# Performance work log

Measured on AMD Instinct MI355X. Metric: run time of the kernel, lower is better.

## Reference

```python
import jax, jax.numpy as jnp
import numpy as np

NUM_BITS = 8
SEQ, BATCH, INPUT, HIDDEN = 512, 256, 256, 256


def fake_quant(w):
    # symmetric per-tensor uniform fake-quantization with straight-through estimator
    qmax = 2.0 ** (NUM_BITS - 1) - 1.0
    scale = jnp.max(jnp.abs(w)) / qmax
    wq = jnp.round(w / scale) * scale
    return w + jax.lax.stop_gradient(wq - w)


def gru_cell(x, h, w_ih, w_hh, b_ih, b_hh):
    # x: [B, I], h: [B, H]; w_ih: [3H, I], w_hh: [3H, H]
    gi = x @ fake_quant(w_ih).T + b_ih  # [B, 3H]
    gh = h @ fake_quant(w_hh).T + b_hh  # [B, 3H]
    i_r, i_z, i_n = jnp.split(gi, 3, axis=-1)
    h_r, h_z, h_n = jnp.split(gh, 3, axis=-1)
    r = jax.nn.sigmoid(i_r + h_r)
    z = jax.nn.sigmoid(i_z + h_z)
    n = jnp.tanh(i_n + r * h_n)
    return (1.0 - z) * n + z * h


def setup_inputs() -> dict:
    key = jax.random.key(0)
    ks = jax.random.split(key, 9)
    s1 = 1.0 / np.sqrt(HIDDEN)
    inp = {
        "x": jax.random.normal(ks[0], (SEQ, BATCH, INPUT), dtype=jnp.float32),
        "h1": jnp.zeros((BATCH, HIDDEN), dtype=jnp.float32),
        "h2": jnp.zeros((BATCH, HIDDEN), dtype=jnp.float32),
        "w_ih1": jax.random.uniform(ks[1], (3 * HIDDEN, INPUT), jnp.float32, -s1, s1),
        "w_hh1": jax.random.uniform(ks[2], (3 * HIDDEN, HIDDEN), jnp.float32, -s1, s1),
        "b_ih1": jax.random.uniform(ks[3], (3 * HIDDEN,), jnp.float32, -s1, s1),
        "b_hh1": jax.random.uniform(ks[4], (3 * HIDDEN,), jnp.float32, -s1, s1),
        "w_ih2": jax.random.uniform(ks[5], (3 * HIDDEN, HIDDEN), jnp.float32, -s1, s1),
        "w_hh2": jax.random.uniform(ks[6], (3 * HIDDEN, HIDDEN), jnp.float32, -s1, s1),
        "b_ih2": jax.random.uniform(ks[7], (3 * HIDDEN,), jnp.float32, -s1, s1),
        "b_hh2": jax.random.uniform(ks[8], (3 * HIDDEN,), jnp.float32, -s1, s1),
    }
    return inp


def reference(x, h1, h2, w_ih1, w_hh1, b_ih1, b_hh1, w_ih2, w_hh2, b_ih2, b_hh2):
    def step(carry, x_t):
        h1, h2 = carry
        h1 = gru_cell(x_t, h1, w_ih1, w_hh1, b_ih1, b_hh1)
        h2 = gru_cell(h1, h2, w_ih2, w_hh2, b_ih2, b_hh2)
        return (h1, h2), None

    (h1, h2), _ = jax.lax.scan(step, (h1, h2), x)
    return h2
```

## Files before the change

kernel.cpp:

```cpp
#include <hip/hip_runtime.h>
#include <hip/hip_fp16.h>
#include <cstdint>

typedef _Float16 half8 __attribute__((ext_vector_type(8)));
typedef _Float16 half4 __attribute__((ext_vector_type(4)));
typedef float f32x4 __attribute__((ext_vector_type(4)));

#define MFMA_F16 __builtin_amdgcn_mfma_f32_16x16x32_f16
#define PIN(x)   asm volatile("" : "+v"(x))
#define LD_RLX(p)   __hip_atomic_load((p),  __ATOMIC_RELAXED, __HIP_MEMORY_SCOPE_AGENT)
#define LD_ACQ(p)   __hip_atomic_load((p),  __ATOMIC_ACQUIRE, __HIP_MEMORY_SCOPE_AGENT)
#define ST_REL(p,v) __hip_atomic_store((p),(v), __ATOMIC_RELEASE, __HIP_MEMORY_SCOPE_AGENT)

__device__ __forceinline__ float fast_rcp(float x){
#if __has_builtin(__builtin_amdgcn_rcpf)
  return __builtin_amdgcn_rcpf(x);
#else
  return 1.0f/x;
#endif
}
__device__ __forceinline__ float fast_exp2(float x){
#if __has_builtin(__builtin_amdgcn_exp2f)
  return __builtin_amdgcn_exp2f(x);
#else
  return exp2f(x);
#endif
}
__device__ __forceinline__ float sigm_f(float x){
  return fast_rcp(1.0f + fast_exp2(-1.44269504f*x));
}
__device__ __forceinline__ float tanh_fast(float x){
  float e = fast_exp2(-2.88539008f*x);
  return fmaf(2.0f, fast_rcp(1.0f + e), -1.0f);
}

__device__ __forceinline__ void bar_weak(){
  asm volatile("s_waitcnt lgkmcnt(0)" ::: "memory");
  __builtin_amdgcn_s_barrier();
  asm volatile("" ::: "memory");
}
__device__ __forceinline__ void bar_strong(){
  asm volatile("s_waitcnt vmcnt(0) lgkmcnt(0)" ::: "memory");
  __builtin_amdgcn_s_barrier();
  asm volatile("" ::: "memory");
}

__global__ __launch_bounds__(256) void k_maxabs(
    const float* __restrict__ w0, const float* __restrict__ w1,
    const float* __restrict__ w2, const float* __restrict__ w3,
    int n, int* __restrict__ slots)
{
  const float* srcs[4] = {w0, w1, w2, w3};
  int m    = blockIdx.x >> 5;
  int part = blockIdx.x & 31;
  const float* w = srcs[m];
  float loc = 0.0f;
  for (int i = part*256 + threadIdx.x; i < n; i += 32*256)
    loc = fmaxf(loc, fabsf(w[i]));
  for (int off = 32; off; off >>= 1)
    loc = fmaxf(loc, __shfl_down(loc, off, 64));
  __shared__ float red[4];
  int wv = threadIdx.x >> 6;
  if ((threadIdx.x & 63) == 0) red[wv] = loc;
  __syncthreads();
  if (threadIdx.x == 0) {
    float mx = fmaxf(fmaxf(red[0], red[1]), fmaxf(red[2], red[3]));
    atomicMax(&slots[m], __float_as_int(mx));
  }
}

__global__ __launch_bounds__(256) void k_quant(
    const float* __restrict__ w0, const float* __restrict__ w1,
    const float* __restrict__ w2, const float* __restrict__ w3,
    const int* __restrict__ slots,
    _Float16* __restrict__ f0, _Float16* __restrict__ f1,
    _Float16* __restrict__ f2, _Float16* __restrict__ f3)
{
  const float* srcs[4] = {w0, w1, w2, w3};
  _Float16*    dsts[4] = {f0, f1, f2, f3};
  int idx = blockIdx.x*256 + threadIdx.x;
  int m = idx / 196608;
  int e = idx - m*196608;
  float scale = __int_as_float(slots[m]) * (1.0f/127.0f);
  float w = srcs[m][e];
  float q = rintf(w/scale) * scale;
  int g = e >> 8, k = e & 255;
  int tile = g >> 4, kb = k >> 5;
  int lane = ((k >> 3) & 3)*16 + (g & 15);
  int off  = (tile*8 + kb)*512 + lane*8 + (k & 7);
  dsts[m][off] = (_Float16)q;
}

__global__ __launch_bounds__(256) void k_xcast(
    const float* __restrict__ x, _Float16* __restrict__ xh)
{
  int n = blockIdx.x*256 + threadIdx.x;
  int t   = n >> 13;
  int rem = n & 8191;
  int bg  = rem >> 5;
  int k8  = rem & 31;
  const float4* src = (const float4*)&x[((size_t)t*256 + bg)*256 + k8*8];
  float4 v0 = src[0], v1 = src[1];
  half8 hv;
  hv[0] = (_Float16)v0.x; hv[1] = (_Float16)v0.y;
  hv[2] = (_Float16)v0.z; hv[3] = (_Float16)v0.w;
  hv[4] = (_Float16)v1.x; hv[5] = (_Float16)v1.y;
  hv[6] = (_Float16)v1.z; hv[7] = (_Float16)v1.w;
  int bb = bg >> 4, b = bg & 15, kb = k8 >> 2, lane = (k8 & 3)*16 + b;
  *(half8*)&xh[(size_t)t*65536 + (size_t)bb*4096 + kb*512 + lane*8] = hv;
}

__global__ __launch_bounds__(512, 1) void k_pipe(
    const _Float16* __restrict__ xh,
    const _Float16* __restrict__ wfih1, const float* __restrict__ bih1,
    _Float16* __restrict__ gi1, const _Float16* __restrict__ wfhh1,
    const float* __restrict__ bhh1, float* __restrict__ hc1,
    _Float16* __restrict__ h1seq,
    const _Float16* __restrict__ wfih2, const float* __restrict__ bih2,
    const float* __restrict__ bhh2, const _Float16* __restrict__ wfhh2,
    float* __restrict__ hc2, _Float16* __restrict__ gi2,
    int* __restrict__ flag0, int* __restrict__ flag1,
    int* __restrict__ flag2, int* __restrict__ flag3)
{
  __shared__ __align__(16) _Float16 hl[2][4096];
  __shared__ __align__(16) _Float16 wn_l[16384];
  const int role = blockIdx.x;
  const int tid  = threadIdx.x;
  const int w = tid >> 6, l = tid & 63, q = l >> 4, c16 = l & 15;

  if (role >= 32) {
    const bool G1 = (role >= 64);
    const int id = G1 ? role - 64 : role - 32;
    const int bb = id >> 1, par = id & 1;
    const _Float16* Wsrc = G1 ? wfih1 : wfih2;
    const float*    bihp = G1 ? bih1  : bih2;
    const float*    bhhp = G1 ? bhh1  : bhh2;
    const _Float16* Asrc = G1 ? xh    : h1seq;
    _Float16*       gout = G1 ? gi1   : gi2;

    float bR[2], bZ[2], bN[2];
    half8 wr[2][8], wz[2][8], wn[2][8];
    #pragma unroll
    for (int nt = 0; nt < 2; nt++) {
      const int j = w*32 + nt*16 + c16;
      bR[nt] = bihp[j]       + bhhp[j];
      bZ[nt] = bihp[256 + j] + bhhp[256 + j];
      bN[nt] = bihp[512 + j];
      const _Float16* WR = Wsrc + (size_t)(2*w + nt)      *4096;
      const _Float16* WZ = Wsrc + (size_t)(16 + 2*w + nt) *4096;
      const _Float16* WN = Wsrc + (size_t)(32 + 2*w + nt) *4096;
      #pragma unroll
      for (int kb = 0; kb < 8; kb++) {
        wr[nt][kb] = *(const half8*)&WR[(kb*64 + l)*8];  PIN(wr[nt][kb]);
        wz[nt][kb] = *(const half8*)&WZ[(kb*64 + l)*8];  PIN(wz[nt][kb]);
        wn[nt][kb] = *(const half8*)&WN[(kb*64 + l)*8];  PIN(wn[nt][kb]);
      }
    }

    for (int g = par; g < 32; g += 2) {
      const int t0 = g*16;
      if (!G1) {
        if (tid == 0) {
          while (LD_RLX(&flag1[bb]) < t0 + 16) __builtin_amdgcn_s_sleep(10);
          if (g >= 4)
            while (LD_RLX(&flag3[bb]) < (g - 3)*16) __builtin_amdgcn_s_sleep(10);
          (void)LD_ACQ(&flag1[bb]);
        }
        __syncthreads();
      }
      for (int t = t0; t < t0 + 16; t++) {
        const _Float16* ap = Asrc + (size_t)t*65536 + (size_t)bb*4096 + l*8;
        f32x4 aR[2], aZ[2], aN[2];
        #pragma unroll
        for (int nt = 0; nt < 2; nt++) {
          aR[nt] = (f32x4){0.f,0.f,0.f,0.f};
          aZ[nt] = (f32x4){0.f,0.f,0.f,0.f};
          aN[nt] = (f32x4){0.f,0.f,0.f,0.f};
        }
        #pragma unroll
        for (int kb = 0; kb < 8; kb++) {
          half8 a = *(const half8*)&ap[kb*512];
          #pragma unroll
          for (int nt = 0; nt < 2; nt++) {
            aR[nt] = MFMA_F16(a, wr[nt][kb], aR[nt], 0, 0, 0);
            aZ[nt] = MFMA_F16(a, wz[nt][kb], aZ[nt], 0, 0, 0);
            aN[nt] = MFMA_F16(a, wn[nt][kb], aN[nt], 0, 0, 0);
          }
        }
        const size_t trow = G1 ? (size_t)t : (size_t)(t & 63);
        #pragma unroll
        for (int nt = 0; nt < 2; nt++) {
          _Float16* op = gout + (trow*256 + (2*w + nt)*16 + bb)*768 + l*12;
          half4 vR, vZ, vN;
          #pragma unroll
          for (int i = 0; i < 4; i++) {
            vR[i] = (_Float16)(aR[nt][i] + bR[nt]);
            vZ[i] = (_Float16)(aZ[nt][i] + bZ[nt]);
            vN[i] = (_Float16)(aN[nt][i] + bN[nt]);
          }
          *(half4*)(op)     = vR;
          *(half4*)(op + 4) = vZ;
          *(half4*)(op + 8) = vN;
        }
      }
      __syncthreads();
      if (tid == 0) {
        if (G1) ST_REL(&flag0[bb*2 + par], t0 + 16);
        else    ST_REL(&flag2[bb*2 + par], t0 + 16);
      }
    }
    return;
  }

  const bool L1 = (role < 16);
  const int bb = L1 ? role : role - 16;
  const int b0 = bb * 16;
  const _Float16* gi = L1 ? gi1 : gi2;
  const _Float16* Wf = L1 ? wfhh1 : wfhh2;
  const float* bhh   = L1 ? bhh1 : bhh2;
  float* hcarry      = L1 ? hc1 : hc2;

  {
    int n = tid*8;
    int b = n >> 8, k = n & 255;
    const float4* s4 = (const float4*)&hcarry[(size_t)(b0 + b)*256 + k];
    float4 v0 = s4[0], v1 = s4[1];
    half8 hv;
    hv[0] = (_Float16)v0.x; hv[1] = (_Float16)v0.y;
    hv[2] = (_Float16)v0.z; hv[3] = (_Float16)v0.w;
    hv[4] = (_Float16)v1.x; hv[5] = (_Float16)v1.y;
    hv[6] = (_Float16)v1.z; hv[7] = (_Float16)v1.w;
    *(half8*)&hl[0][(k >> 5)*512 + (((k >> 3) & 3)*16 + b)*8] = hv;
  }

  float bN[2];
  float hprev[2][4];
  half8 wr[2][8], wz[2][8], wn[2][6];
  int   wr_off[2];
  int   gil[2];
  #pragma unroll
  for (int nt = 0; nt < 2; nt++) {
    const int j = w*32 + nt*16 + c16;
    bN[nt] = bhh[512 + j];
    #pragma unroll
    for (int i = 0; i < 4; i++)
      hprev[nt][i] = hcarry[(size_t)(b0 + q*4 + i)*256 + j];
    const _Float16* WR = Wf + (size_t)(2*w + nt)      *4096;
    const _Float16* WZ = Wf + (size_t)(16 + 2*w + nt) *4096;
    const _Float16* WN = Wf + (size_t)(32 + 2*w + nt) *4096;
    #pragma unroll
    for (int kb = 0; kb < 8; kb++) {
      wr[nt][kb] = *(const half8*)&WR[(kb*64 + l)*8];  PIN(wr[nt][kb]);
      wz[nt][kb] = *(const half8*)&WZ[(kb*64 + l)*8];  PIN(wz[nt][kb]);
    }
    #pragma unroll
    for (int kb = 2; kb < 8; kb++) {
      wn[nt][kb-2] = *(const half8*)&WN[(kb*64 + l)*8];  PIN(wn[nt][kb-2]);
    }
    #pragma unroll
    for (int kb = 0; kb < 2; kb++)
      *(half8*)&wn_l[((w*2 + nt)*2 + kb)*512 + l*8] =
          *(const half8*)&WN[(kb*64 + l)*8];
    wr_off[nt] = (j >> 5)*512 + ((j >> 3) & 3)*128 + (j & 7);
    gil[nt]    = ((2*w + nt)*16 + bb)*768 + l*12;
  }
  _Float16* hq = L1 ? (h1seq + (size_t)bb*4096 + tid*8) : (_Float16*)nullptr;

  __syncthreads();
  half4 pR[2], pZ[2], pN[2];
  int cur = 0;
  for (int t = 0; t < 512; t++) {
    if ((t & 15) == 0) {
      if (tid == 0) {
        int* f = L1 ? &flag0[bb*2 + ((t >> 4) & 1)]
                    : &flag2[bb*2 + ((t >> 4) & 1)];
        while (LD_RLX(f) < t + 16) __builtin_amdgcn_s_sleep(10);
        (void)LD_ACQ(f);
      }
      __syncthreads();
      const int tm = L1 ? t : (t & 63);
      const _Float16* gbase = gi + (size_t)tm*196608;
      #pragma unroll
      for (int nt = 0; nt < 2; nt++) {
        const _Float16* gp = gbase + gil[nt];
        pR[nt] = *(const half4*)(gp);
        pZ[nt] = *(const half4*)(gp + 4);
        pN[nt] = *(const half4*)(gp + 8);
      }
    }
    half4 vR[2], vZ[2], vN[2];
    #pragma unroll
    for (int nt = 0; nt < 2; nt++) {
      vR[nt] = pR[nt]; vZ[nt] = pZ[nt]; vN[nt] = pN[nt];
    }

    f32x4 aR[2], aZ[2], aN[2];
    #pragma unroll
    for (int nt = 0; nt < 2; nt++) {
      aR[nt] = (f32x4){0.f,0.f,0.f,0.f};
      aZ[nt] = (f32x4){0.f,0.f,0.f,0.f};
      aN[nt] = (f32x4){0.f,0.f,0.f,0.f};
    }
    #pragma unroll
    for (int kb = 0; kb < 8; kb++) {
      half8 a = *(const half8*)&hl[cur][kb*512 + l*8];
      #pragma unroll
      for (int nt = 0; nt < 2; nt++) {
        half8 bn = (kb < 2)
            ? *(const half8*)&wn_l[((w*2 + nt)*2 + kb)*512 + l*8]
            : wn[nt][kb-2];
        aR[nt] = MFMA_F16(a, wr[nt][kb], aR[nt], 0, 0, 0);
        aZ[nt] = MFMA_F16(a, wz[nt][kb], aZ[nt], 0, 0, 0);
        aN[nt] = MFMA_F16(a, bn,         aN[nt], 0, 0, 0);
      }
    }

    if (((t + 1) & 15) != 0) {
      const int tn = L1 ? (t + 1) : ((t + 1) & 63);
      const _Float16* gbase = gi + (size_t)tn*196608;
      #pragma unroll
      for (int nt = 0; nt < 2; nt++) {
        const _Float16* gp = gbase + gil[nt];
        pR[nt] = *(const half4*)(gp);
        pZ[nt] = *(const half4*)(gp + 4);
        pN[nt] = *(const half4*)(gp + 8);
      }
    }

    const int nxt = cur ^ 1;
    #pragma unroll
    for (int nt = 0; nt < 2; nt++) {
      #pragma unroll
      for (int i = 0; i < 4; i++) {
        float r  = sigm_f(aR[nt][i] + (float)vR[nt][i]);
        float z  = sigm_f(aZ[nt][i] + (float)vZ[nt][i]);
        float nn = tanh_fast((float)vN[nt][i] + r*(aN[nt][i] + bN[nt]));
        float hp = nn + z*(hprev[nt][i] - nn);
        hprev[nt][i] = hp;
        hl[nxt][wr_off[nt] + (q*4 + i)*8] = (_Float16)hp;
      }
    }

    if ((t & 15) == 0 && t > 0) {
      bar_strong();
      if (tid == 0) {
        if (L1) ST_REL(&flag1[bb], t);
        else    ST_REL(&flag3[bb], t);
      }
    } else {
      bar_weak();
    }
    if (L1)
      *(half8*)&hq[(size_t)t*65536] = *(const half8*)&hl[nxt][tid*8];
    cur = nxt;
  }
  bar_strong();
  if (tid == 0) {
    if (L1) ST_REL(&flag1[bb], 512);
    else    ST_REL(&flag3[bb], 512);
  }

  #pragma unroll
  for (int nt = 0; nt < 2; nt++) {
    const int j = w*32 + nt*16 + c16;
    #pragma unroll
    for (int i = 0; i < 4; i++)
      hcarry[(size_t)(b0 + q*4 + i)*256 + j] = hprev[nt][i];
  }
}

extern "C" void kernel_launch(void* const* d_in, const int* in_sizes, int n_in,
                              void* d_out, int out_size, void* d_ws, size_t ws_size,
                              hipStream_t stream)
{
  const float* x     = (const float*)d_in[0];
  const float* h1_0  = (const float*)d_in[1];
  const float* h2_0  = (const float*)d_in[2];
  const float* w_ih1 = (const float*)d_in[3];
  const float* w_hh1 = (const float*)d_in[4];
  const float* b_ih1 = (const float*)d_in[5];
  const float* b_hh1 = (const float*)d_in[6];
  const float* w_ih2 = (const float*)d_in[7];
  const float* w_hh2 = (const float*)d_in[8];
  const float* b_ih2 = (const float*)d_in[9];
  const float* b_hh2 = (const float*)d_in[10];

  char* ws = (char*)d_ws;
  size_t off = 0;
  auto alloc = [&](size_t bytes) -> void* {
    void* p = ws + off; off += (bytes + 255) & ~(size_t)255; return p;
  };
  int*      slots   = (int*)     alloc(16);
  _Float16* wf_ih1  = (_Float16*)alloc(196608*2);
  _Float16* wf_hh1  = (_Float16*)alloc(196608*2);
  _Float16* wf_ih2  = (_Float16*)alloc(196608*2);
  _Float16* wf_hh2  = (_Float16*)alloc(196608*2);
  float*    hc1     = (float*)   alloc(256*256*4);
  float*    hc2     = (float*)   alloc(256*256*4);
  int*      flag0   = (int*)     alloc(32*4);
  int*      flag1   = (int*)     alloc(16*4);
  int*      flag2   = (int*)     alloc(32*4);
  int*      flag3   = (int*)     alloc(16*4);
  _Float16* gi1     = (_Float16*)alloc((size_t)512*393216);
  _Float16* h1seq   = (_Float16*)alloc((size_t)512*131072);
  _Float16* gi2     = (_Float16*)alloc((size_t)64*393216);
  _Float16* xhbuf   = (_Float16*)alloc((size_t)512*131072);

  k_maxabs<<<128, 256, 0, stream>>>(w_ih1, w_hh1, w_ih2, w_hh2, 196608, slots);
  k_quant <<<3072, 256, 0, stream>>>(w_ih1, w_hh1, w_ih2, w_hh2, slots,
                                     wf_ih1, wf_hh1, wf_ih2, wf_hh2);
  k_xcast <<<16384, 256, 0, stream>>>(x, xhbuf);
  (void)hipMemcpyAsync(hc1, h1_0, 256*256*4, hipMemcpyDeviceToDevice, stream);
  (void)hipMemcpyAsync(hc2, h2_0, 256*256*4, hipMemcpyDeviceToDevice, stream);

  k_pipe<<<96, 512, 0, stream>>>(xhbuf, wf_ih1, b_ih1, gi1, wf_hh1, b_hh1,
                                 hc1, h1seq, wf_ih2, b_ih2, b_hh2, wf_hh2,
                                 hc2, gi2, flag0, flag1, flag2, flag3);

  (void)hipMemcpyAsync(d_out, hc2, 256*256*4, hipMemcpyDeviceToDevice, stream);
}
```

Baseline: 1.341 ms.

## Fuse weight quantization into pipe kernel and ring-buffer layer-1 input gates

Removes the separate quantization kernel: each block now reads fp32 weights and quantizes its MFMA fragments in registers at load time. The layer-1 input-projection buffer shrinks from the full sequence to a 64-step ring. This requires new flow control so the G1 producers wait on layer-1 consumer progress, as G2 already did. It also raises launch_bounds min blocks to 2, which may constrain register allocation for the large pinned weight arrays. The goal is to cut one launch and the gi1 memory footprint and traffic, in exchange for extra producer stalls and uncoalesced fp32 weight reads at startup.

```diff
diff --git a/kernel.cpp b/kernel.cpp
--- a/kernel.cpp
+++ b/kernel.cpp
@@ -43,6 +43,24 @@
   asm volatile("s_waitcnt vmcnt(0) lgkmcnt(0)" ::: "memory");
   __builtin_amdgcn_s_barrier();
   asm volatile("" ::: "memory");
+}
+
+__device__ __forceinline__ half8 qfrag(const float* __restrict__ W, int tile,
+                                       int kb, int l, float scale){
+  int row = tile*16 + (l & 15);
+  int k0  = kb*32 + (l >> 4)*8;
+  const float4* p = (const float4*)&W[row*256 + k0];
+  float4 a = p[0], b = p[1];
+  half8 h;
+  h[0] = (_Float16)(rintf(a.x/scale)*scale);
+  h[1] = (_Float16)(rintf(a.y/scale)*scale);
+  h[2] = (_Float16)(rintf(a.z/scale)*scale);
+  h[3] = (_Float16)(rintf(a.w/scale)*scale);
+  h[4] = (_Float16)(rintf(b.x/scale)*scale);
+  h[5] = (_Float16)(rintf(b.y/scale)*scale);
+  h[6] = (_Float16)(rintf(b.z/scale)*scale);
+  h[7] = (_Float16)(rintf(b.w/scale)*scale);
+  return h;
 }
 
 __global__ __launch_bounds__(256) void k_maxabs(
@@ -69,28 +87,6 @@
   }
 }
 
-__global__ __launch_bounds__(256) void k_quant(
-    const float* __restrict__ w0, const float* __restrict__ w1,
-    const float* __restrict__ w2, const float* __restrict__ w3,
-    const int* __restrict__ slots,
-    _Float16* __restrict__ f0, _Float16* __restrict__ f1,
-    _Float16* __restrict__ f2, _Float16* __restrict__ f3)
-{
-  const float* srcs[4] = {w0, w1, w2, w3};
-  _Float16*    dsts[4] = {f0, f1, f2, f3};
-  int idx = blockIdx.x*256 + threadIdx.x;
-  int m = idx / 196608;
-  int e = idx - m*196608;
-  float scale = __int_as_float(slots[m]) * (1.0f/127.0f);
-  float w = srcs[m][e];
-  float q = rintf(w/scale) * scale;
-  int g = e >> 8, k = e & 255;
-  int tile = g >> 4, kb = k >> 5;
-  int lane = ((k >> 3) & 3)*16 + (g & 15);
-  int off  = (tile*8 + kb)*512 + lane*8 + (k & 7);
-  dsts[m][off] = (_Float16)q;
-}
-
 __global__ __launch_bounds__(256) void k_xcast(
     const float* __restrict__ x, _Float16* __restrict__ xh)
 {
@@ -110,15 +106,16 @@
   *(half8*)&xh[(size_t)t*65536 + (size_t)bb*4096 + kb*512 + lane*8] = hv;
 }
 
-__global__ __launch_bounds__(512, 1) void k_pipe(
+__global__ __launch_bounds__(512, 2) void k_pipe(
     const _Float16* __restrict__ xh,
-    const _Float16* __restrict__ wfih1, const float* __restrict__ bih1,
-    _Float16* __restrict__ gi1, const _Float16* __restrict__ wfhh1,
+    const float* __restrict__ wih1, const float* __restrict__ bih1,
+    _Float16* __restrict__ gi1, const float* __restrict__ whh1,
     const float* __restrict__ bhh1, float* __restrict__ hc1,
     _Float16* __restrict__ h1seq,
-    const _Float16* __restrict__ wfih2, const float* __restrict__ bih2,
-    const float* __restrict__ bhh2, const _Float16* __restrict__ wfhh2,
+    const float* __restrict__ wih2, const float* __restrict__ bih2,
+    const float* __restrict__ bhh2, const float* __restrict__ whh2,
     float* __restrict__ hc2, _Float16* __restrict__ gi2,
+    const int* __restrict__ slots,
     int* __restrict__ flag0, int* __restrict__ flag1,
     int* __restrict__ flag2, int* __restrict__ flag3)
 {
@@ -132,11 +129,12 @@
     const bool G1 = (role >= 64);
     const int id = G1 ? role - 64 : role - 32;
     const int bb = id >> 1, par = id & 1;
-    const _Float16* Wsrc = G1 ? wfih1 : wfih2;
+    const float*    Wsrc = G1 ? wih1  : wih2;
     const float*    bihp = G1 ? bih1  : bih2;
     const float*    bhhp = G1 ? bhh1  : bhh2;
     const _Float16* Asrc = G1 ? xh    : h1seq;
     _Float16*       gout = G1 ? gi1   : gi2;
+    const float sc = __int_as_float(slots[G1 ? 0 : 2]) * (1.0f/127.0f);
 
     float bR[2], bZ[2], bN[2];
     half8 wr[2][8], wz[2][8], wn[2][8];
@@ -146,28 +144,28 @@
       bR[nt] = bihp[j]       + bhhp[j];
       bZ[nt] = bihp[256 + j] + bhhp[256 + j];
       bN[nt] = bihp[512 + j];
-      const _Float16* WR = Wsrc + (size_t)(2*w + nt)      *4096;
-      const _Float16* WZ = Wsrc + (size_t)(16 + 2*w + nt) *4096;
-      const _Float16* WN = Wsrc + (size_t)(32 + 2*w + nt) *4096;
       #pragma unroll
       for (int kb = 0; kb < 8; kb++) {
-        wr[nt][kb] = *(const half8*)&WR[(kb*64 + l)*8];  PIN(wr[nt][kb]);
-        wz[nt][kb] = *(const half8*)&WZ[(kb*64 + l)*8];  PIN(wz[nt][kb]);
-        wn[nt][kb] = *(const half8*)&WN[(kb*64 + l)*8];  PIN(wn[nt][kb]);
+        wr[nt][kb] = qfrag(Wsrc,      2*w + nt, kb, l, sc);  PIN(wr[nt][kb]);
+        wz[nt][kb] = qfrag(Wsrc, 16 + 2*w + nt, kb, l, sc);  PIN(wz[nt][kb]);
+        wn[nt][kb] = qfrag(Wsrc, 32 + 2*w + nt, kb, l, sc);  PIN(wn[nt][kb]);
       }
     }
 
     for (int g = par; g < 32; g += 2) {
       const int t0 = g*16;
-      if (!G1) {
-        if (tid == 0) {
+      if (tid == 0) {
+        if (!G1) {
           while (LD_RLX(&flag1[bb]) < t0 + 16) __builtin_amdgcn_s_sleep(10);
           if (g >= 4)
             while (LD_RLX(&flag3[bb]) < (g - 3)*16) __builtin_amdgcn_s_sleep(10);
           (void)LD_ACQ(&flag1[bb]);
+        } else if (g >= 4) {
+          while (LD_RLX(&flag1[bb]) < (g - 3)*16) __builtin_amdgcn_s_sleep(10);
+          (void)LD_ACQ(&flag1[bb]);
         }
-        __syncthreads();
-      }
+      }
+      __syncthreads();
       for (int t = t0; t < t0 + 16; t++) {
         const _Float16* ap = Asrc + (size_t)t*65536 + (size_t)bb*4096 + l*8;
         f32x4 aR[2], aZ[2], aN[2];
@@ -187,7 +185,7 @@
             aN[nt] = MFMA_F16(a, wn[nt][kb], aN[nt], 0, 0, 0);
           }
         }
-        const size_t trow = G1 ? (size_t)t : (size_t)(t & 63);
+        const size_t trow = (size_t)(t & 63);
         #pragma unroll
         for (int nt = 0; nt < 2; nt++) {
           _Float16* op = gout + (trow*256 + (2*w + nt)*16 + bb)*768 + l*12;
@@ -216,9 +214,10 @@
   const int bb = L1 ? role : role - 16;
   const int b0 = bb * 16;
   const _Float16* gi = L1 ? gi1 : gi2;
-  const _Float16* Wf = L1 ? wfhh1 : wfhh2;
+  const float* Wf    = L1 ? whh1 : whh2;
   const float* bhh   = L1 ? bhh1 : bhh2;
   float* hcarry      = L1 ? hc1 : hc2;
+  const float sc     = __int_as_float(slots[L1 ? 1 : 3]) * (1.0f/127.0f);
 
   {
     int n = tid*8;
@@ -245,22 +244,19 @@
     #pragma unroll
     for (int i = 0; i < 4; i++)
       hprev[nt][i] = hcarry[(size_t)(b0 + q*4 + i)*256 + j];
-    const _Float16* WR = Wf + (size_t)(2*w + nt)      *4096;
-    const _Float16* WZ = Wf + (size_t)(16 + 2*w + nt) *4096;
-    const _Float16* WN = Wf + (size_t)(32 + 2*w + nt) *4096;
     #pragma unroll
     for (int kb = 0; kb < 8; kb++) {
-      wr[nt][kb] = *(const half8*)&WR[(kb*64 + l)*8];  PIN(wr[nt][kb]);
-      wz[nt][kb] = *(const half8*)&WZ[(kb*64 + l)*8];  PIN(wz[nt][kb]);
+      wr[nt][kb] = qfrag(Wf,      2*w + nt, kb, l, sc);  PIN(wr[nt][kb]);
+      wz[nt][kb] = qfrag(Wf, 16 + 2*w + nt, kb, l, sc);  PIN(wz[nt][kb]);
     }
     #pragma unroll
     for (int kb = 2; kb < 8; kb++) {
-      wn[nt][kb-2] = *(const half8*)&WN[(kb*64 + l)*8];  PIN(wn[nt][kb-2]);
+      wn[nt][kb-2] = qfrag(Wf, 32 + 2*w + nt, kb, l, sc);  PIN(wn[nt][kb-2]);
     }
     #pragma unroll
     for (int kb = 0; kb < 2; kb++)
       *(half8*)&wn_l[((w*2 + nt)*2 + kb)*512 + l*8] =
-          *(const half8*)&WN[(kb*64 + l)*8];
+          qfrag(Wf, 32 + 2*w + nt, kb, l, sc);
     wr_off[nt] = (j >> 5)*512 + ((j >> 3) & 3)*128 + (j & 7);
     gil[nt]    = ((2*w + nt)*16 + bb)*768 + l*12;
   }
@@ -278,7 +274,7 @@
         (void)LD_ACQ(f);
       }
       __syncthreads();
-      const int tm = L1 ? t : (t & 63);
+      const int tm = t & 63;
       const _Float16* gbase = gi + (size_t)tm*196608;
       #pragma unroll
       for (int nt = 0; nt < 2; nt++) {
@@ -316,7 +312,7 @@
     }
 
     if (((t + 1) & 15) != 0) {
-      const int tn = L1 ? (t + 1) : ((t + 1) & 63);
+      const int tn = (t + 1) & 63;
       const _Float16* gbase = gi + (size_t)tn*196608;
       #pragma unroll
       for (int nt = 0; nt < 2; nt++) {
@@ -391,31 +387,25 @@
     void* p = ws + off; off += (bytes + 255) & ~(size_t)255; return p;
   };
   int*      slots   = (int*)     alloc(16);
-  _Float16* wf_ih1  = (_Float16*)alloc(196608*2);
-  _Float16* wf_hh1  = (_Float16*)alloc(196608*2);
-  _Float16* wf_ih2  = (_Float16*)alloc(196608*2);
-  _Float16* wf_hh2  = (_Float16*)alloc(196608*2);
   float*    hc1     = (float*)   alloc(256*256*4);
   float*    hc2     = (float*)   alloc(256*256*4);
   int*      flag0   = (int*)     alloc(32*4);
   int*      flag1   = (int*)     alloc(16*4);
   int*      flag2   = (int*)     alloc(32*4);
   int*      flag3   = (int*)     alloc(16*4);
-  _Float16* gi1     = (_Float16*)alloc((size_t)512*393216);
+  _Float16* gi1     = (_Float16*)alloc((size_t)64*393216);
   _Float16* h1seq   = (_Float16*)alloc((size_t)512*131072);
   _Float16* gi2     = (_Float16*)alloc((size_t)64*393216);
   _Float16* xhbuf   = (_Float16*)alloc((size_t)512*131072);
 
   k_maxabs<<<128, 256, 0, stream>>>(w_ih1, w_hh1, w_ih2, w_hh2, 196608, slots);
-  k_quant <<<3072, 256, 0, stream>>>(w_ih1, w_hh1, w_ih2, w_hh2, slots,
-                                     wf_ih1, wf_hh1, wf_ih2, wf_hh2);
   k_xcast <<<16384, 256, 0, stream>>>(x, xhbuf);
   (void)hipMemcpyAsync(hc1, h1_0, 256*256*4, hipMemcpyDeviceToDevice, stream);
   (void)hipMemcpyAsync(hc2, h2_0, 256*256*4, hipMemcpyDeviceToDevice, stream);
 
-  k_pipe<<<96, 512, 0, stream>>>(xhbuf, wf_ih1, b_ih1, gi1, wf_hh1, b_hh1,
-                                 hc1, h1seq, wf_ih2, b_ih2, b_hh2, wf_hh2,
-                                 hc2, gi2, flag0, flag1, flag2, flag3);
+  k_pipe<<<96, 512, 0, stream>>>(xhbuf, w_ih1, b_ih1, gi1, w_hh1, b_hh1,
+                                 hc1, h1seq, w_ih2, b_ih2, b_hh2, w_hh2,
+                                 hc2, gi2, slots, flag0, flag1, flag2, flag3);
 
   (void)hipMemcpyAsync(d_out, hc2, 256*256*4, hipMemcpyDeviceToDevice, stream);
 }
```

Result: no change. 1.338 ms (-0.2%).
